# Kernel optimization log

Measured on AMD Instinct MI355X. Metric: run time of the kernel, lower is better.

Reference implementation:

```python
import jax, jax.numpy as jnp
import numpy as np

ALPHA = 0.2  # LeakyReLU negative slope


def _gat_layer(h, dst, adj, w, a_in, a_out, b):
    # h: [N, F_in], dst: [N, K] int (edge (i,k): i -> dst[i,k]), adj: [N, K]
    hid = h @ w                      # [N, D]
    s_in = hid @ a_in                # [N]  (attention applied to source-node half)
    s_out = hid @ a_out              # [N]  (attention applied to dest-node half)
    # edge scores, grouped per source node (matches view(-1, num_neighs) softmax)
    e = jax.nn.leaky_relu(s_in[:, None] + s_out[dst], ALPHA)   # [N, K]
    # torch code detaches attention (Variable(..., requires_grad=False))
    att = jax.lax.stop_gradient(jax.nn.softmax(e, axis=1))     # [N, K]
    w_edge = adj * att                                          # [N, K]
    # SpMM: out[i] = sum_k w_edge[i,k] * hid[dst[i,k]]
    out = jnp.einsum('nk,nkd->nd', w_edge, hid[dst]) + b        # [N, D]
    return out


def setup_inputs() -> dict:
    key = jax.random.key(0)
    ks = jax.random.split(key, 12)
    N, K, F, H, O = 100000, 16, 128, 128, 128
    stdv1 = 1.0 / np.sqrt(H)
    stdv2 = 1.0 / np.sqrt(O)
    u = lambda k, shp, s: jax.random.uniform(k, shp, jnp.float32, -s, s)
    return {
        'x': jax.random.normal(ks[0], (N, F), jnp.float32),
        'dst_idx': jax.random.randint(ks[1], (N, K), 0, N),
        'adj_vals': jax.random.uniform(ks[2], (N, K), jnp.float32),
        'w1': u(ks[3], (F, H), stdv1),
        'a_in1': jax.random.normal(ks[4], (H,), jnp.float32) * (1.414 / np.sqrt(H)),
        'a_out1': jax.random.normal(ks[5], (H,), jnp.float32) * (1.414 / np.sqrt(H)),
        'b1': u(ks[6], (H,), stdv1),
        'w2': u(ks[7], (H, O), stdv2),
        'a_in2': jax.random.normal(ks[8], (O,), jnp.float32) * (1.414 / np.sqrt(O)),
        'a_out2': jax.random.normal(ks[9], (O,), jnp.float32) * (1.414 / np.sqrt(O)),
        'b2': u(ks[10], (O,), stdv2),
    }


def reference(x, dst_idx, adj_vals, w1, a_in1, a_out1, b1, w2, a_in2, a_out2, b2):
    h = jax.nn.relu(_gat_layer(x, dst_idx, adj_vals, w1, a_in1, a_out1, b1))
    h = jax.nn.relu(_gat_layer(h, dst_idx, adj_vals, w2, a_in2, a_out2, b2))
    return h
```

## Files before the change

### kernel.cpp

```cpp
#include <hip/hip_runtime.h>

#define ALPHA 0.2f
#define LDA 136

typedef short bf16x8 __attribute__((ext_vector_type(8)));
typedef float f32x4  __attribute__((ext_vector_type(4)));

static __device__ __forceinline__ float bf2f(unsigned short u) {
    union { unsigned int i; float f; } v; v.i = ((unsigned int)u) << 16; return v.f;
}
static __device__ __forceinline__ unsigned short f2bf(float f) {
    union { float f; unsigned int i; } v; v.f = f;
    unsigned int x = v.i;
    return (unsigned short)((x + 0x7fffu + ((x >> 16) & 1u)) >> 16);
}
static __device__ __forceinline__ float bflo(int u) {
    union { unsigned int i; float f; } v; v.i = ((unsigned int)u) << 16; return v.f;
}
static __device__ __forceinline__ float bfhi(int u) {
    union { unsigned int i; float f; } v; v.i = ((unsigned int)u) & 0xffff0000u; return v.f;
}
static __device__ __forceinline__ void acc8(float* a, const int4 hv, const float w) {
    a[0] = fmaf(w, bflo(hv.x), a[0]); a[1] = fmaf(w, bfhi(hv.x), a[1]);
    a[2] = fmaf(w, bflo(hv.y), a[2]); a[3] = fmaf(w, bfhi(hv.y), a[3]);
    a[4] = fmaf(w, bflo(hv.z), a[4]); a[5] = fmaf(w, bfhi(hv.z), a[5]);
    a[6] = fmaf(w, bflo(hv.w), a[6]); a[7] = fmaf(w, bfhi(hv.w), a[7]);
}

__global__ __launch_bounds__(128)
void prep_wT_kernel(const float* __restrict__ w1, const float* __restrict__ w2,
                    unsigned short* __restrict__ wT1, unsigned short* __restrict__ wT2)
{
    const int b = blockIdx.x;
    const float* w = (b >> 4) ? w2 : w1;
    unsigned short* wT = (b >> 4) ? wT2 : wT1;
    const int k0 = (b & 15) * 8;
    const int c = threadIdx.x;

    ushort4 u0, u1;
    u0.x = f2bf(w[(k0 + 0) * 128 + c]); u0.y = f2bf(w[(k0 + 1) * 128 + c]);
    u0.z = f2bf(w[(k0 + 2) * 128 + c]); u0.w = f2bf(w[(k0 + 3) * 128 + c]);
    u1.x = f2bf(w[(k0 + 4) * 128 + c]); u1.y = f2bf(w[(k0 + 5) * 128 + c]);
    u1.z = f2bf(w[(k0 + 6) * 128 + c]); u1.w = f2bf(w[(k0 + 7) * 128 + c]);
    *(ushort4*)&wT[c * 128 + k0]     = u0;
    *(ushort4*)&wT[c * 128 + k0 + 4] = u1;
}

__global__ __launch_bounds__(256, 4)
void gemm_score_mfma(const float* __restrict__ src,
                     const unsigned short* __restrict__ wT,
                     const float* __restrict__ a_in,
                     const float* __restrict__ a_out,
                     unsigned short* __restrict__ hid,
                     float* __restrict__ s_in,
                     float* __restrict__ s_out,
                     int n)
{
    __shared__ short Bs[128 * LDA];
    __shared__ float aS[2][128];

    const int tid  = threadIdx.x;
    const int lane = tid & 63;
    const int wv   = tid >> 6;
    const int m    = lane & 15;
    const int q    = lane >> 4;
    const int rbase = blockIdx.x * 64;
    const int row   = rbase + wv * 16 + m;
    const bool rok  = (row < n);

    if (tid < 128) { aS[0][tid] = a_in[tid]; aS[1][tid] = a_out[tid]; }

    bf16x8 aF[4];
    {
        const float* p = &src[(size_t)row * 128 + q * 8];
        #pragma unroll
        for (int ks = 0; ks < 4; ks++) {
            if (rok) {
                float4 v0 = *(const float4*)(p + ks * 32);
                float4 v1 = *(const float4*)(p + ks * 32 + 4);
                bf16x8 a;
                a[0] = (short)f2bf(v0.x); a[1] = (short)f2bf(v0.y);
                a[2] = (short)f2bf(v0.z); a[3] = (short)f2bf(v0.w);
                a[4] = (short)f2bf(v1.x); a[5] = (short)f2bf(v1.y);
                a[6] = (short)f2bf(v1.z); a[7] = (short)f2bf(v1.w);
                aF[ks] = a;
            } else aF[ks] = (bf16x8){0,0,0,0,0,0,0,0};
        }
    }

    #pragma unroll
    for (int i = 0; i < 8; i++) {
        int e = tid + i * 256;
        int nr = e >> 4, j = (e & 15) * 8;
        int4 v = *(const int4*)&wT[nr * 128 + j];
        *(int4*)&Bs[nr * LDA + j] = v;
    }
    __syncthreads();

    f32x4 acc[8];
    #pragma unroll
    for (int t = 0; t < 8; t++) acc[t] = (f32x4){0.f, 0.f, 0.f, 0.f};

    const short* Bbase = &Bs[m * LDA + q * 8];
    #pragma unroll
    for (int ks = 0; ks < 4; ks++) {
        #pragma unroll
        for (int t = 0; t < 8; t++) {
            bf16x8 bF = *(const bf16x8*)(Bbase + t * 16 * LDA + ks * 32);
            acc[t] = __builtin_amdgcn_mfma_f32_16x16x32_bf16(aF[ks], bF, acc[t], 0, 0, 0);
        }
    }

    float pin[4] = {0.f, 0.f, 0.f, 0.f}, pout[4] = {0.f, 0.f, 0.f, 0.f};
    #pragma unroll
    for (int t = 0; t < 8; t++) {
        float ai = aS[0][t * 16 + m];
        float ao = aS[1][t * 16 + m];
        #pragma unroll
        for (int r = 0; r < 4; r++) {
            pin[r]  += acc[t][r] * ai;
            pout[r] += acc[t][r] * ao;
        }
    }
    #pragma unroll
    for (int msk = 8; msk >= 1; msk >>= 1) {
        #pragma unroll
        for (int r = 0; r < 4; r++) {
            pin[r]  += __shfl_xor(pin[r],  msk);
            pout[r] += __shfl_xor(pout[r], msk);
        }
    }
    if (m == 0) {
        #pragma unroll
        for (int r = 0; r < 4; r++) {
            int g = rbase + wv * 16 + q * 4 + r;
            if (g < n) { s_in[g] = pin[r]; s_out[g] = pout[r]; }
        }
    }

    __syncthreads();
    short* Es = Bs;
    #pragma unroll
    for (int t = 0; t < 8; t++)
        #pragma unroll
        for (int r = 0; r < 4; r++)
            Es[(wv * 16 + q * 4 + r) * LDA + t * 16 + m] = (short)f2bf(acc[t][r]);
    __syncthreads();
    #pragma unroll
    for (int i = 0; i < 4; i++) {
        int e = tid + i * 256;
        int r = e >> 4, j = (e & 15) * 8;
        int gr = rbase + r;
        if (gr < n) {
            int4 v = *(const int4*)&Es[r * LDA + j];
            *(int4*)&hid[(size_t)gr * 128 + j] = v;
        }
    }
}

__global__ __launch_bounds__(256, 4)
void fused_agg_gemm(const unsigned short* __restrict__ hid1,
                    const float* __restrict__ s_in1,
                    const float* __restrict__ s_out1,
                    const int* __restrict__ dst,
                    const float* __restrict__ adj,
                    const float* __restrict__ bias1,
                    const unsigned short* __restrict__ wT2,
                    const float* __restrict__ a_in2,
                    const float* __restrict__ a_out2,
                    unsigned short* __restrict__ hid2,
                    float* __restrict__ s_in2,
                    float* __restrict__ s_out2,
                    int n)
{
    __shared__ short As[64 * LDA];
    __shared__ short Bs[64 * LDA];
    __shared__ float aS[2][128];

    const int tid  = threadIdx.x;
    const int lane = tid & 63;
    const int wv   = tid >> 6;
    const int rbase = blockIdx.x * 64;

    if (tid < 128) { aS[0][tid] = a_in2[tid]; aS[1][tid] = a_out2[tid]; }

    #pragma unroll
    for (int i = 0; i < 4; i++) {
        int e = tid + i * 256;
        int nr = e >> 4, j = (e & 15) * 8;
        int4 v = *(const int4*)&wT2[nr * 128 + j];
        *(int4*)&Bs[nr * LDA + j] = v;
    }

    const int jn  = lane >> 2;
    const int kq  = lane & 3;
    const int node = rbase + wv * 16 + jn;
    const bool nok = (node < n);

    int4   dk4 = make_int4(0, 0, 0, 0);
    float4 av4 = make_float4(0.f, 0.f, 0.f, 0.f);
    float  si  = 0.f;
    if (nok) {
        dk4 = *(const int4*)&dst[node * 16 + kq * 4];
        av4 = *(const float4*)&adj[node * 16 + kq * 4];
        si  = s_in1[node];
    }
    float e0 = si + s_out1[dk4.x], e1 = si + s_out1[dk4.y];
    float e2 = si + s_out1[dk4.z], e3 = si + s_out1[dk4.w];
    e0 = (e0 > 0.f) ? e0 : ALPHA * e0;  e1 = (e1 > 0.f) ? e1 : ALPHA * e1;
    e2 = (e2 > 0.f) ? e2 : ALPHA * e2;  e3 = (e3 > 0.f) ? e3 : ALPHA * e3;
    float mx = fmaxf(fmaxf(e0, e1), fmaxf(e2, e3));
    mx = fmaxf(mx, __shfl_xor(mx, 1));
    mx = fmaxf(mx, __shfl_xor(mx, 2));
    float p0 = __expf(e0 - mx), p1 = __expf(e1 - mx);
    float p2 = __expf(e2 - mx), p3 = __expf(e3 - mx);
    float sm = p0 + p1 + p2 + p3;
    sm += __shfl_xor(sm, 1);
    sm += __shfl_xor(sm, 2);
    const float inv = __frcp_rn(sm);

    {
        short* rowp = &As[(wv * 16 + jn) * LDA];
        int4 pa = make_int4(dk4.x, __float_as_int(av4.x * p0 * inv),
                            dk4.y, __float_as_int(av4.y * p1 * inv));
        int4 pb = make_int4(dk4.z, __float_as_int(av4.z * p2 * inv),
                            dk4.w, __float_as_int(av4.w * p3 * inv));
        *(int4*)(rowp + kq * 16)     = pa;
        *(int4*)(rowp + kq * 16 + 8) = pb;
    }

    const int m = lane & 15;
    const int q = lane >> 4;
    {
        const float4 bb0 = *(const float4*)&bias1[m * 8];
        const float4 bb1 = *(const float4*)&bias1[m * 8 + 4];
        #pragma unroll
        for (int jj = 0; jj < 4; jj++) {
            const int rloc = wv * 16 + jj * 4 + q;
            const short* trow = &As[rloc * LDA];
            float acc[8] = {0.f, 0.f, 0.f, 0.f, 0.f, 0.f, 0.f, 0.f};
            #pragma unroll
            for (int k2 = 0; k2 < 8; k2++) {
                const int4 pp  = *(const int4*)(trow + k2 * 8);
                const int4 hv0 = *(const int4*)&hid1[((size_t)(unsigned)pp.x << 7) + (m << 3)];
                const int4 hv1 = *(const int4*)&hid1[((size_t)(unsigned)pp.z << 7) + (m << 3)];
                acc8(acc, hv0, __int_as_float(pp.y));
                acc8(acc, hv1, __int_as_float(pp.w));
            }
            const float r0 = fmaxf(acc[0] + bb0.x, 0.f);
            const float r1 = fmaxf(acc[1] + bb0.y, 0.f);
            const float r2 = fmaxf(acc[2] + bb0.z, 0.f);
            const float r3 = fmaxf(acc[3] + bb0.w, 0.f);
            const float r4 = fmaxf(acc[4] + bb1.x, 0.f);
            const float r5 = fmaxf(acc[5] + bb1.y, 0.f);
            const float r6 = fmaxf(acc[6] + bb1.z, 0.f);
            const float r7 = fmaxf(acc[7] + bb1.w, 0.f);
            int4 ov;
            ov.x = (int)f2bf(r0) | ((int)f2bf(r1) << 16);
            ov.y = (int)f2bf(r2) | ((int)f2bf(r3) << 16);
            ov.z = (int)f2bf(r4) | ((int)f2bf(r5) << 16);
            ov.w = (int)f2bf(r6) | ((int)f2bf(r7) << 16);
            *(int4*)&As[rloc * LDA + m * 8] = ov;
        }
    }
    __syncthreads();

    bf16x8 aF[4];
    {
        const short* Abase = &As[(wv * 16 + m) * LDA + q * 8];
        #pragma unroll
        for (int ks = 0; ks < 4; ks++)
            aF[ks] = *(const bf16x8*)(Abase + ks * 32);
    }

    f32x4 acc[8];
    #pragma unroll
    for (int t = 0; t < 8; t++) acc[t] = (f32x4){0.f, 0.f, 0.f, 0.f};

    const short* Bbase = &Bs[m * LDA + q * 8];
    #pragma unroll
    for (int ks = 0; ks < 4; ks++) {
        #pragma unroll
        for (int t = 0; t < 4; t++) {
            bf16x8 bF = *(const bf16x8*)(Bbase + t * 16 * LDA + ks * 32);
            acc[t] = __builtin_amdgcn_mfma_f32_16x16x32_bf16(aF[ks], bF, acc[t], 0, 0, 0);
        }
    }
    __syncthreads();
    #pragma unroll
    for (int i = 0; i < 4; i++) {
        int e = tid + i * 256;
        int nr = e >> 4, j = (e & 15) * 8;
        int4 v = *(const int4*)&wT2[(64 + nr) * 128 + j];
        *(int4*)&Bs[nr * LDA + j] = v;
    }
    __syncthreads();
    #pragma unroll
    for (int ks = 0; ks < 4; ks++) {
        #pragma unroll
        for (int t = 4; t < 8; t++) {
            bf16x8 bF = *(const bf16x8*)(Bbase + (t - 4) * 16 * LDA + ks * 32);
            acc[t] = __builtin_amdgcn_mfma_f32_16x16x32_bf16(aF[ks], bF, acc[t], 0, 0, 0);
        }
    }

    float pin[4] = {0.f, 0.f, 0.f, 0.f}, pout[4] = {0.f, 0.f, 0.f, 0.f};
    #pragma unroll
    for (int t = 0; t < 8; t++) {
        float ai = aS[0][t * 16 + m];
        float ao = aS[1][t * 16 + m];
        #pragma unroll
        for (int r = 0; r < 4; r++) {
            pin[r]  += acc[t][r] * ai;
            pout[r] += acc[t][r] * ao;
        }
    }
    #pragma unroll
    for (int msk = 8; msk >= 1; msk >>= 1) {
        #pragma unroll
        for (int r = 0; r < 4; r++) {
            pin[r]  += __shfl_xor(pin[r],  msk);
            pout[r] += __shfl_xor(pout[r], msk);
        }
    }
    if (m == 0) {
        #pragma unroll
        for (int r = 0; r < 4; r++) {
            int g = rbase + wv * 16 + q * 4 + r;
            if (g < n) { s_in2[g] = pin[r]; s_out2[g] = pout[r]; }
        }
    }

    __syncthreads();
    short* Es = As;
    #pragma unroll
    for (int t = 0; t < 8; t++)
        #pragma unroll
        for (int r = 0; r < 4; r++)
            Es[(wv * 16 + q * 4 + r) * LDA + t * 16 + m] = (short)f2bf(acc[t][r]);
    __syncthreads();
    #pragma unroll
    for (int i = 0; i < 4; i++) {
        int e = tid + i * 256;
        int r = e >> 4, j = (e & 15) * 8;
        int gr = rbase + r;
        if (gr < n) {
            int4 v = *(const int4*)&Es[r * LDA + j];
            *(int4*)&hid2[(size_t)gr * 128 + j] = v;
        }
    }
}

__global__ __launch_bounds__(256, 4)
void gat_aggregate_final(const unsigned short* __restrict__ hid,
                         const float* __restrict__ s_in,
                         const float* __restrict__ s_out,
                         const int* __restrict__ dst,
                         const float* __restrict__ adj,
                         const float* __restrict__ bias,
                         float* __restrict__ out,
                         int n)
{
    __shared__ __align__(16) int2 tbl[64][18];
    const int tid  = threadIdx.x;
    const int lane = tid & 63;
    const int wv   = tid >> 6;
    const int rbase = blockIdx.x * 64;

    const int jn  = lane >> 2;
    const int kq  = lane & 3;
    const int node = rbase + wv * 16 + jn;
    const bool nok = (node < n);

    int4   dk4 = make_int4(0, 0, 0, 0);
    float4 av4 = make_float4(0.f, 0.f, 0.f, 0.f);
    float  si  = 0.f;
    if (nok) {
        dk4 = *(const int4*)&dst[node * 16 + kq * 4];
        av4 = *(const float4*)&adj[node * 16 + kq * 4];
        si  = s_in[node];
    }
    float e0 = si + s_out[dk4.x], e1 = si + s_out[dk4.y];
    float e2 = si + s_out[dk4.z], e3 = si + s_out[dk4.w];
    e0 = (e0 > 0.f) ? e0 : ALPHA * e0;  e1 = (e1 > 0.f) ? e1 : ALPHA * e1;
    e2 = (e2 > 0.f) ? e2 : ALPHA * e2;  e3 = (e3 > 0.f) ? e3 : ALPHA * e3;
    float mx = fmaxf(fmaxf(e0, e1), fmaxf(e2, e3));
    mx = fmaxf(mx, __shfl_xor(mx, 1));
    mx = fmaxf(mx, __shfl_xor(mx, 2));
    float p0 = __expf(e0 - mx), p1 = __expf(e1 - mx);
    float p2 = __expf(e2 - mx), p3 = __expf(e3 - mx);
    float sm = p0 + p1 + p2 + p3;
    sm += __shfl_xor(sm, 1);
    sm += __shfl_xor(sm, 2);
    const float inv = __frcp_rn(sm);

    {
        int4 pa = make_int4(dk4.x, __float_as_int(av4.x * p0 * inv),
                            dk4.y, __float_as_int(av4.y * p1 * inv));
        int4 pb = make_int4(dk4.z, __float_as_int(av4.z * p2 * inv),
                            dk4.w, __float_as_int(av4.w * p3 * inv));
        *(int4*)&tbl[wv * 16 + jn][kq * 4]     = pa;
        *(int4*)&tbl[wv * 16 + jn][kq * 4 + 2] = pb;
    }

    const int m = lane & 15;
    const int q = lane >> 4;
    const float4 bb0 = *(const float4*)&bias[m * 8];
    const float4 bb1 = *(const float4*)&bias[m * 8 + 4];

    #pragma unroll
    for (int jj = 0; jj < 4; jj++) {
        const int rl = wv * 16 + jj * 4 + q;
        const int nodeg = rbase + rl;
        float acc[8] = {0.f, 0.f, 0.f, 0.f, 0.f, 0.f, 0.f, 0.f};
        #pragma unroll
        for (int k2 = 0; k2 < 8; k2++) {
            const int4 pp  = *(const int4*)&tbl[rl][k2 * 2];
            const int4 hv0 = *(const int4*)&hid[((size_t)(unsigned)pp.x << 7) + (m << 3)];
            const int4 hv1 = *(const int4*)&hid[((size_t)(unsigned)pp.z << 7) + (m << 3)];
            acc8(acc, hv0, __int_as_float(pp.y));
            acc8(acc, hv1, __int_as_float(pp.w));
        }
        if (nodeg < n) {
            float4 o0, o1;
            o0.x = fmaxf(acc[0] + bb0.x, 0.f);
            o0.y = fmaxf(acc[1] + bb0.y, 0.f);
            o0.z = fmaxf(acc[2] + bb0.z, 0.f);
            o0.w = fmaxf(acc[3] + bb0.w, 0.f);
            o1.x = fmaxf(acc[4] + bb1.x, 0.f);
            o1.y = fmaxf(acc[5] + bb1.y, 0.f);
            o1.z = fmaxf(acc[6] + bb1.z, 0.f);
            o1.w = fmaxf(acc[7] + bb1.w, 0.f);
            float* op = &out[(size_t)nodeg * 128 + m * 8];
            *(float4*)op       = o0;
            *(float4*)(op + 4) = o1;
        }
    }
}

extern "C" void kernel_launch(void* const* d_in, const int* in_sizes, int n_in,
                              void* d_out, int out_size, void* d_ws, size_t ws_size,
                              hipStream_t stream)
{
    const float* x      = (const float*)d_in[0];
    const int*   dst    = (const int*)d_in[1];
    const float* adj    = (const float*)d_in[2];
    const float* w1     = (const float*)d_in[3];
    const float* a_in1  = (const float*)d_in[4];
    const float* a_out1 = (const float*)d_in[5];
    const float* b1     = (const float*)d_in[6];
    const float* w2     = (const float*)d_in[7];
    const float* a_in2  = (const float*)d_in[8];
    const float* a_out2 = (const float*)d_in[9];
    const float* b2     = (const float*)d_in[10];

    const int N = in_sizes[0] / 128;

    unsigned short* hid2  = (unsigned short*)d_ws;
    float*          s_in1 = (float*)(hid2 + (size_t)N * 128);
    float*          s_out1= s_in1 + N;
    float*          s_in2 = s_out1 + N;
    float*          s_out2= s_in2 + N;
    unsigned short* wT1   = (unsigned short*)(s_out2 + N);
    unsigned short* wT2   = wT1 + 128 * 128;
    unsigned short* hid1  = (unsigned short*)d_out + out_size;

    dim3 blk(256);
    dim3 ggrid((N + 63) / 64);

    prep_wT_kernel<<<32, 128, 0, stream>>>(w1, w2, wT1, wT2);

    gemm_score_mfma<<<ggrid, blk, 0, stream>>>(x, wT1, a_in1, a_out1,
                                               hid1, s_in1, s_out1, N);
    fused_agg_gemm<<<ggrid, blk, 0, stream>>>(hid1, s_in1, s_out1, dst, adj, b1,
                                              wT2, a_in2, a_out2,
                                              hid2, s_in2, s_out2, N);
    gat_aggregate_final<<<ggrid, blk, 0, stream>>>(hid2, s_in2, s_out2, dst, adj,
                                                   b2, (float*)d_out, N);
}
```

Before: 252.4 us.

## Prepack weights into MFMA fragment order and read them directly from global memory

The prep kernel now writes both bf16 weight matrices in the per-lane MFMA B-fragment order. The two GEMM kernels load B fragments straight from global or L2 memory instead of staging the weights in LDS. This removes the LDS weight tiles, their copy loops and several barriers, which cuts LDS use. The launch-bound occupancy hints are raised to match. The cost is that every block repeats 32 global vector loads per wave for the weights, which rely on cache hits, and the higher occupancy targets may force register spills.

```diff
diff --git a/kernel.cpp b/kernel.cpp
--- a/kernel.cpp
+++ b/kernel.cpp
@@ -27,28 +27,32 @@
     a[6] = fmaf(w, bflo(hv.w), a[6]); a[7] = fmaf(w, bfhi(hv.w), a[7]);
 }
 
-__global__ __launch_bounds__(128)
-void prep_wT_kernel(const float* __restrict__ w1, const float* __restrict__ w2,
-                    unsigned short* __restrict__ wT1, unsigned short* __restrict__ wT2)
+__global__ __launch_bounds__(64)
+void prep_wT_frag(const float* __restrict__ w1, const float* __restrict__ w2,
+                  unsigned short* __restrict__ wT1f, unsigned short* __restrict__ wT2f)
 {
     const int b = blockIdx.x;
-    const float* w = (b >> 4) ? w2 : w1;
-    unsigned short* wT = (b >> 4) ? wT2 : wT1;
-    const int k0 = (b & 15) * 8;
-    const int c = threadIdx.x;
+    const float* w = (b >> 5) ? w2 : w1;
+    unsigned short* wf = (b >> 5) ? wT2f : wT1f;
+    const int u = b & 31;
+    const int t = u >> 2, ks = u & 3;
+    const int lane = threadIdx.x;
+    const int m = lane & 15, q = lane >> 4;
+    const int c  = t * 16 + m;
+    const int k0 = ks * 32 + q * 8;
 
     ushort4 u0, u1;
     u0.x = f2bf(w[(k0 + 0) * 128 + c]); u0.y = f2bf(w[(k0 + 1) * 128 + c]);
     u0.z = f2bf(w[(k0 + 2) * 128 + c]); u0.w = f2bf(w[(k0 + 3) * 128 + c]);
     u1.x = f2bf(w[(k0 + 4) * 128 + c]); u1.y = f2bf(w[(k0 + 5) * 128 + c]);
     u1.z = f2bf(w[(k0 + 6) * 128 + c]); u1.w = f2bf(w[(k0 + 7) * 128 + c]);
-    *(ushort4*)&wT[c * 128 + k0]     = u0;
-    *(ushort4*)&wT[c * 128 + k0 + 4] = u1;
-}
-
-__global__ __launch_bounds__(256, 4)
+    *(ushort4*)&wf[(u * 64 + lane) * 8]     = u0;
+    *(ushort4*)&wf[(u * 64 + lane) * 8 + 4] = u1;
+}
+
+__global__ __launch_bounds__(256, 6)
 void gemm_score_mfma(const float* __restrict__ src,
-                     const unsigned short* __restrict__ wT,
+                     const unsigned short* __restrict__ wTf,
                      const float* __restrict__ a_in,
                      const float* __restrict__ a_out,
                      unsigned short* __restrict__ hid,
@@ -56,7 +60,7 @@
                      float* __restrict__ s_out,
                      int n)
 {
-    __shared__ short Bs[128 * LDA];
+    __shared__ short Es[64 * LDA];
     __shared__ float aS[2][128];
 
     const int tid  = threadIdx.x;
@@ -87,26 +91,18 @@
             } else aF[ks] = (bf16x8){0,0,0,0,0,0,0,0};
         }
     }
-
-    #pragma unroll
-    for (int i = 0; i < 8; i++) {
-        int e = tid + i * 256;
-        int nr = e >> 4, j = (e & 15) * 8;
-        int4 v = *(const int4*)&wT[nr * 128 + j];
-        *(int4*)&Bs[nr * LDA + j] = v;
-    }
     __syncthreads();
 
     f32x4 acc[8];
     #pragma unroll
     for (int t = 0; t < 8; t++) acc[t] = (f32x4){0.f, 0.f, 0.f, 0.f};
 
-    const short* Bbase = &Bs[m * LDA + q * 8];
+    const bf16x8* Bf = (const bf16x8*)wTf;
     #pragma unroll
     for (int ks = 0; ks < 4; ks++) {
         #pragma unroll
         for (int t = 0; t < 8; t++) {
-            bf16x8 bF = *(const bf16x8*)(Bbase + t * 16 * LDA + ks * 32);
+            bf16x8 bF = Bf[(t * 4 + ks) * 64 + lane];
             acc[t] = __builtin_amdgcn_mfma_f32_16x16x32_bf16(aF[ks], bF, acc[t], 0, 0, 0);
         }
     }
@@ -138,8 +134,6 @@
         }
     }
 
-    __syncthreads();
-    short* Es = Bs;
     #pragma unroll
     for (int t = 0; t < 8; t++)
         #pragma unroll
@@ -158,14 +152,14 @@
     }
 }
 
-__global__ __launch_bounds__(256, 4)
+__global__ __launch_bounds__(256, 8)
 void fused_agg_gemm(const unsigned short* __restrict__ hid1,
                     const float* __restrict__ s_in1,
                     const float* __restrict__ s_out1,
                     const int* __restrict__ dst,
                     const float* __restrict__ adj,
                     const float* __restrict__ bias1,
-                    const unsigned short* __restrict__ wT2,
+                    const unsigned short* __restrict__ wT2f,
                     const float* __restrict__ a_in2,
                     const float* __restrict__ a_out2,
                     unsigned short* __restrict__ hid2,
@@ -174,7 +168,6 @@
                     int n)
 {
     __shared__ short As[64 * LDA];
-    __shared__ short Bs[64 * LDA];
     __shared__ float aS[2][128];
 
     const int tid  = threadIdx.x;
@@ -183,14 +176,6 @@
     const int rbase = blockIdx.x * 64;
 
     if (tid < 128) { aS[0][tid] = a_in2[tid]; aS[1][tid] = a_out2[tid]; }
-
-    #pragma unroll
-    for (int i = 0; i < 4; i++) {
-        int e = tid + i * 256;
-        int nr = e >> 4, j = (e & 15) * 8;
-        int4 v = *(const int4*)&wT2[nr * 128 + j];
-        *(int4*)&Bs[nr * LDA + j] = v;
-    }
 
     const int jn  = lane >> 2;
     const int kq  = lane & 3;
@@ -277,29 +262,12 @@
     #pragma unroll
     for (int t = 0; t < 8; t++) acc[t] = (f32x4){0.f, 0.f, 0.f, 0.f};
 
-    const short* Bbase = &Bs[m * LDA + q * 8];
+    const bf16x8* Bf = (const bf16x8*)wT2f;
     #pragma unroll
     for (int ks = 0; ks < 4; ks++) {
         #pragma unroll
-        for (int t = 0; t < 4; t++) {
-            bf16x8 bF = *(const bf16x8*)(Bbase + t * 16 * LDA + ks * 32);
-            acc[t] = __builtin_amdgcn_mfma_f32_16x16x32_bf16(aF[ks], bF, acc[t], 0, 0, 0);
-        }
-    }
-    __syncthreads();
-    #pragma unroll
-    for (int i = 0; i < 4; i++) {
-        int e = tid + i * 256;
-        int nr = e >> 4, j = (e & 15) * 8;
-        int4 v = *(const int4*)&wT2[(64 + nr) * 128 + j];
-        *(int4*)&Bs[nr * LDA + j] = v;
-    }
-    __syncthreads();
-    #pragma unroll
-    for (int ks = 0; ks < 4; ks++) {
-        #pragma unroll
-        for (int t = 4; t < 8; t++) {
-            bf16x8 bF = *(const bf16x8*)(Bbase + (t - 4) * 16 * LDA + ks * 32);
+        for (int t = 0; t < 8; t++) {
+            bf16x8 bF = Bf[(t * 4 + ks) * 64 + lane];
             acc[t] = __builtin_amdgcn_mfma_f32_16x16x32_bf16(aF[ks], bF, acc[t], 0, 0, 0);
         }
     }
@@ -331,13 +299,12 @@
         }
     }
 
-    __syncthreads();
-    short* Es = As;
+    short* Eo = As;
     #pragma unroll
     for (int t = 0; t < 8; t++)
         #pragma unroll
         for (int r = 0; r < 4; r++)
-            Es[(wv * 16 + q * 4 + r) * LDA + t * 16 + m] = (short)f2bf(acc[t][r]);
+            Eo[(wv * 16 + q * 4 + r) * LDA + t * 16 + m] = (short)f2bf(acc[t][r]);
     __syncthreads();
     #pragma unroll
     for (int i = 0; i < 4; i++) {
@@ -345,13 +312,13 @@
         int r = e >> 4, j = (e & 15) * 8;
         int gr = rbase + r;
         if (gr < n) {
-            int4 v = *(const int4*)&Es[r * LDA + j];
+            int4 v = *(const int4*)&Eo[r * LDA + j];
             *(int4*)&hid2[(size_t)gr * 128 + j] = v;
         }
     }
 }
 
-__global__ __launch_bounds__(256, 4)
+__global__ __launch_bounds__(256, 8)
 void gat_aggregate_final(const unsigned short* __restrict__ hid,
                          const float* __restrict__ s_in,
                          const float* __restrict__ s_out,
@@ -362,6 +329,7 @@
                          int n)
 {
     __shared__ __align__(16) int2 tbl[64][18];
+
     const int tid  = threadIdx.x;
     const int lane = tid & 63;
     const int wv   = tid >> 6;
@@ -461,19 +429,19 @@
     float*          s_out1= s_in1 + N;
     float*          s_in2 = s_out1 + N;
     float*          s_out2= s_in2 + N;
-    unsigned short* wT1   = (unsigned short*)(s_out2 + N);
-    unsigned short* wT2   = wT1 + 128 * 128;
+    unsigned short* wT1f  = (unsigned short*)(s_out2 + N);
+    unsigned short* wT2f  = wT1f + 128 * 128;
     unsigned short* hid1  = (unsigned short*)d_out + out_size;
 
     dim3 blk(256);
     dim3 ggrid((N + 63) / 64);
 
-    prep_wT_kernel<<<32, 128, 0, stream>>>(w1, w2, wT1, wT2);
-
-    gemm_score_mfma<<<ggrid, blk, 0, stream>>>(x, wT1, a_in1, a_out1,
+    prep_wT_frag<<<64, 64, 0, stream>>>(w1, w2, wT1f, wT2f);
+
+    gemm_score_mfma<<<ggrid, blk, 0, stream>>>(x, wT1f, a_in1, a_out1,
                                                hid1, s_in1, s_out1, N);
     fused_agg_gemm<<<ggrid, blk, 0, stream>>>(hid1, s_in1, s_out1, dst, adj, b1,
-                                              wT2, a_in2, a_out2,
+                                              wT2f, a_in2, a_out2,
                                               hid2, s_in2, s_out2, N);
     gat_aggregate_final<<<ggrid, blk, 0, stream>>>(hid2, s_in2, s_out2, dst, adj,
                                                    b2, (float*)d_out, N);
```

Result: slower. 526.3 us (+108.5%).
